# Performance work log

Measured on AMD Instinct MI355X. Metric: run time of the kernel, lower is better.

## Reference

```python
import jax, jax.numpy as jnp
import numpy as np

B, K, D = 8192, 8192, 512


def setup_inputs() -> dict:
    key = jax.random.key(0)
    k1, k2 = jax.random.split(key)
    previous_residual = jax.random.normal(k1, (B, D), dtype=jnp.float32)
    codebook_embeddings = jax.random.normal(k2, (K, D), dtype=jnp.float32)
    return {"previous_residual": previous_residual,
            "codebook_embeddings": codebook_embeddings}


def reference(previous_residual, codebook_embeddings):
    # Squared Euclidean distances [B, K] via the expansion
    # subtract+square+sum, without materializing the [B, K, D] intermediate).
    x_sq = jnp.sum(previous_residual * previous_residual, axis=-1, keepdims=True)   # [B, 1]
    e_sq = jnp.sum(codebook_embeddings * codebook_embeddings, axis=-1)              # [K]
    cross = jnp.einsum('bd,kd->bk', previous_residual, codebook_embeddings)         # [B, K]
    distances = x_sq - 2.0 * cross + e_sq[None, :]                                  # [B, K]
    closest_codebook_index = jnp.argmin(distances, axis=1)                          # [B] int
    codebook_embedding = codebook_embeddings[closest_codebook_index]                # [B, D] gather
    next_residual = previous_residual - codebook_embedding                          # [B, D]
    return closest_codebook_index, next_residual
```

## Files before the change

kernel.cpp:

```cpp
#include <hip/hip_runtime.h>

#define Bn 8192
#define Kn 8192
#define Dn 512
#define WINDOW 0.25f

typedef _Float16 half8 __attribute__((ext_vector_type(8)));
typedef float floatx4 __attribute__((ext_vector_type(4)));
typedef unsigned long long u64;

__device__ __forceinline__ unsigned int fkey(float f) {
    unsigned int u = __float_as_uint(f);
    return (u & 0x80000000u) ? ~u : (u | 0x80000000u);
}

__device__ __forceinline__ void gld16(const _Float16* g, _Float16* l) {
    __builtin_amdgcn_global_load_lds(
        (const __attribute__((address_space(1))) unsigned int*)g,
        (__attribute__((address_space(3))) unsigned int*)l, 16, 0, 0);
}

__global__ __launch_bounds__(256) void esq_kernel(const float* __restrict__ E,
                                                  float* __restrict__ esq) {
    int wave = threadIdx.x >> 6;
    int lane = threadIdx.x & 63;
    int k = blockIdx.x * 4 + wave;
    const float4* row = (const float4*)(E + (size_t)k * Dn);
    float4 v0 = row[lane];
    float4 v1 = row[64 + lane];
    float s = v0.x*v0.x + v0.y*v0.y + v0.z*v0.z + v0.w*v0.w
            + v1.x*v1.x + v1.y*v1.y + v1.z*v1.z + v1.w*v1.w;
    #pragma unroll
    for (int off = 32; off > 0; off >>= 1) s += __shfl_down(s, off, 64);
    if (lane == 0) esq[k] = s;
}

__global__ __launch_bounds__(256) void convert_hi(
    const float* __restrict__ X, const float* __restrict__ E,
    _Float16* __restrict__ Xh, _Float16* __restrict__ Eh,
    float* __restrict__ esq)
{
    const bool isE = blockIdx.x >= 1024;
    const int pc = blockIdx.x & 1023;
    const int panel = pc >> 4;
    const int chunk = pc & 15;
    const float* src = isE ? E : X;
    _Float16* dst = isE ? Eh : Xh;
    const int t = threadIdx.x;
    const int row = t >> 1;
    const int kh  = (t & 1) * 16;
    const float* p = &src[(size_t)(panel * 128 + row) * Dn + chunk * 32 + kh];
    float4 v[4];
    v[0] = *(const float4*)(p + 0);
    v[1] = *(const float4*)(p + 4);
    v[2] = *(const float4*)(p + 8);
    v[3] = *(const float4*)(p + 12);
    const int slotbase = ((row >> 6) << 8) + (((row >> 4) & 3) << 6) + (row & 15);
    #pragma unroll
    for (int j = 0; j < 2; ++j) {
        half8 h;
        #pragma unroll
        for (int q = 0; q < 2; ++q) {
            const float4 w = v[j * 2 + q];
            h[q*4+0]=(_Float16)w.x; h[q*4+1]=(_Float16)w.y;
            h[q*4+2]=(_Float16)w.z; h[q*4+3]=(_Float16)w.w;
        }
        const int kq = (t & 1) * 2 + j;
        const size_t off = ((size_t)(panel * 16 + chunk) * 512
                            + slotbase + kq * 16) * 8;
        *(half8*)&dst[off] = h;
    }
    if (isE) {
        float s = 0.f;
        #pragma unroll
        for (int i = 0; i < 4; ++i)
            s += v[i].x*v[i].x + v[i].y*v[i].y + v[i].z*v[i].z + v[i].w*v[i].w;
        s += __shfl_xor(s, 1);
        if ((t & 1) == 0) atomicAdd(&esq[panel * 128 + row], s);
    }
}

__global__ __launch_bounds__(256, 2) void argmin_hi(
    const _Float16* __restrict__ Xh, const _Float16* __restrict__ Eh,
    const float* __restrict__ esq, float* __restrict__ bestf)
{
    __shared__ __align__(16) _Float16 sX[2][8192];
    __shared__ __align__(16) _Float16 sE[2][8192];

    const int tid  = threadIdx.x;
    const int bid  = blockIdx.x;
    const int lid  = bid >> 3;
    const int rg   = (bid & 7) | ((lid & 1) << 3);
    const int mb   = lid >> 1;
    const int m0   = mb * 128, n0 = rg * 512;
    const int lane = tid & 63, wave = tid >> 6;
    const int wx   = wave & 1, wy = wave >> 1;
    const int colg = lane & 15, quad = lane >> 4;

    float v1[16], v2[16];
    #pragma unroll
    for (int i = 0; i < 16; ++i) { v1[i] = INFINITY; v2[i] = INFINITY; }

    const _Float16* gX  = Xh + (size_t)mb * 65536 + tid * 8;
    const _Float16* gE0 = Eh + (size_t)(rg * 4) * 65536 + tid * 8;
    const int aoff = wy * 2048 + lane * 8;
    const int boff = wx * 2048 + lane * 8;
    const unsigned colg4 = (unsigned)colg << 4;

    auto stage = [&](int cc, int b) {
        const _Float16* sx = gX + (cc & 7) * 8192;
        const _Float16* se = gE0 + (size_t)(cc >> 3) * 65536 + (cc & 7) * 8192;
        _Float16* dX = &sX[b][tid * 8];
        _Float16* dE = &sE[b][tid * 8];
        #pragma unroll
        for (int j = 0; j < 4; ++j) gld16(sx + j * 2048, dX + j * 2048);
        #pragma unroll
        for (int j = 0; j < 4; ++j) gld16(se + j * 2048, dE + j * 2048);
    };

    floatx4 acc[4][4];

    auto compute = [&](int b) {
        #pragma unroll
        for (int s = 0; s < 2; ++s) {
            const int so = s * 4096;
            half8 bh[4];
            #pragma unroll
            for (int ni = 0; ni < 4; ++ni)
                bh[ni] = *(const half8*)&sE[b][boff + so + ni * 512];
            #pragma unroll
            for (int mi = 0; mi < 4; ++mi) {
                half8 ah = *(const half8*)&sX[b][aoff + so + mi * 512];
                #pragma unroll
                for (int ni = 0; ni < 4; ++ni)
                    acc[mi][ni] = __builtin_amdgcn_mfma_f32_16x16x32_f16(
                        ah, bh[ni], acc[mi][ni], 0, 0, 0);
            }
        }
    };

    stage(0, 0);
    asm volatile("s_waitcnt vmcnt(0)" ::: "memory");
    __builtin_amdgcn_s_barrier();

    for (int nt = 0; nt < 4; ++nt) {
        #pragma unroll
        for (int i = 0; i < 4; ++i)
            #pragma unroll
            for (int j = 0; j < 4; ++j) acc[i][j] = {0.f, 0.f, 0.f, 0.f};

        for (int c2 = 0; c2 < 4; ++c2) {
            const int cc0 = nt * 8 + c2 * 2;
            stage(cc0 + 1, 1);
            compute(0);
            asm volatile("s_waitcnt vmcnt(0)" ::: "memory");
            __builtin_amdgcn_s_barrier();
            if (cc0 + 2 < 32) stage(cc0 + 2, 0);
            compute(1);
            asm volatile("s_waitcnt vmcnt(0)" ::: "memory");
            __builtin_amdgcn_s_barrier();
        }

        float eqv[4];
        #pragma unroll
        for (int ni = 0; ni < 4; ++ni)
            eqv[ni] = esq[n0 + nt * 128 + wx * 64 + ni * 16 + colg];
        #pragma unroll
        for (int mi = 0; mi < 4; ++mi)
            #pragma unroll
            for (int r = 0; r < 4; ++r) {
                const int i = mi * 4 + r;
                #pragma unroll
                for (int ni = 0; ni < 4; ++ni) {
                    const float dv = eqv[ni] - 2.0f * acc[mi][ni][r];
                    const unsigned ob = colg4 | (unsigned)((nt << 2) | ni);
                    const float key = __uint_as_float(
                        (__float_as_uint(dv) & 0xFFFFFF00u) | ob);
                    v2[i] = fminf(v2[i], fmaxf(v1[i], key));
                    v1[i] = fminf(v1[i], key);
                }
            }
    }

    #pragma unroll
    for (int mi = 0; mi < 4; ++mi)
        #pragma unroll
        for (int r = 0; r < 4; ++r) {
            const int i = mi * 4 + r;
            float a1 = v1[i], a2 = v2[i];
            #pragma unroll
            for (int off = 1; off < 16; off <<= 1) {
                const float p1 = __shfl_xor(a1, off);
                const float p2 = __shfl_xor(a2, off);
                a2 = fminf(fmaxf(a1, p1), fminf(a2, p2));
                a1 = fminf(a1, p1);
            }
            if (colg == 0) {
                const int row = m0 + wy * 64 + mi * 16 + quad * 4 + r;
                float2 st; st.x = a1; st.y = a2;
                *(float2*)&bestf[(size_t)row * 64 + rg * 4 + wx * 2] = st;
            }
        }
}

__global__ __launch_bounds__(256) void refine_kernel(
    const float* __restrict__ X, const float* __restrict__ E,
    const float* __restrict__ bestf, float* __restrict__ out)
{
    const int lane = threadIdx.x & 63, wave = threadIdx.x >> 6;
    const int b = blockIdx.x * 4 + wave;

    const float val = bestf[(size_t)b * 64 + lane];
    const unsigned bits = __float_as_uint(val);
    const int rg = lane >> 2, wx = (lane >> 1) & 1;
    const int colg = (bits >> 4) & 15, nt = (bits >> 2) & 3, ni = bits & 3;
    const int col = rg * 512 + nt * 128 + wx * 64 + ni * 16 + colg;

    float mn = val;
    #pragma unroll
    for (int off = 1; off < 64; off <<= 1) mn = fminf(mn, __shfl_xor(mn, off));

    const float4* xr = (const float4*)(X + (size_t)b * Dn);
    const float4 x0 = xr[lane * 2], x1 = xr[lane * 2 + 1];

    u64 bestk = ~0ull;
    u64 mask = __ballot(val <= mn + WINDOW);
    while (mask) {
        const int s = __builtin_ctzll(mask);
        mask &= mask - 1;
        const int c = __shfl(col, s);
        const float4* er = (const float4*)(E + (size_t)c * Dn);
        const float4 e0 = er[lane * 2], e1 = er[lane * 2 + 1];
        float p = e0.x*(e0.x - 2.f*x0.x) + e0.y*(e0.y - 2.f*x0.y)
                + e0.z*(e0.z - 2.f*x0.z) + e0.w*(e0.w - 2.f*x0.w)
                + e1.x*(e1.x - 2.f*x1.x) + e1.y*(e1.y - 2.f*x1.y)
                + e1.z*(e1.z - 2.f*x1.z) + e1.w*(e1.w - 2.f*x1.w);
        #pragma unroll
        for (int off = 1; off < 64; off <<= 1) p += __shfl_xor(p, off);
        const u64 k = ((u64)fkey(p) << 32) | (u64)(unsigned int)c;
        if (k < bestk) bestk = k;
    }

    const int idx = (int)(unsigned int)(bestk & 0xFFFFFFFFull);
    if (lane == 0) out[b] = (float)idx;
    const float4* er = (const float4*)(E + (size_t)idx * Dn);
    const float4 e0 = er[lane * 2], e1 = er[lane * 2 + 1];
    float4 r0, r1;
    r0.x = x0.x - e0.x; r0.y = x0.y - e0.y; r0.z = x0.z - e0.z; r0.w = x0.w - e0.w;
    r1.x = x1.x - e1.x; r1.y = x1.y - e1.y; r1.z = x1.z - e1.z; r1.w = x1.w - e1.w;
    float4* o = (float4*)(out + Bn + (size_t)b * Dn);
    o[lane * 2] = r0; o[lane * 2 + 1] = r1;
}

#define KSPLIT 16
#define LDSW 132
__global__ __launch_bounds__(256, 2) void argmin_fp32(
    const float* __restrict__ X, const float* __restrict__ E,
    const float* __restrict__ esq, u64* __restrict__ best)
{
    __shared__ __align__(16) float Xs[16][LDSW];
    __shared__ __align__(16) float Es[16][LDSW];
    __shared__ u64 red[128][16];
    const int tid = threadIdx.x;
    const int tx = tid & 15, ty = tid >> 4;
    const int rowTile = blockIdx.x / KSPLIT;
    const int split   = blockIdx.x % KSPLIT;
    const int m0 = rowTile * 128;
    const int kbase = split * (Kn / KSPLIT);
    float bestv[8]; int besti[8];
    #pragma unroll
    for (int i = 0; i < 8; ++i) { bestv[i] = INFINITY; besti[i] = 0; }
    const int ldRow = tid >> 2, ldD = (tid & 3) * 4;
    for (int kt = 0; kt < (Kn / KSPLIT) / 128; ++kt) {
        const int k0 = kbase + kt * 128;
        float acc[8][8] = {};
        for (int dc = 0; dc < Dn / 16; ++dc) {
            const int d0 = dc * 16;
            float4 xa = *(const float4*)&X[(size_t)(m0 + ldRow)      * Dn + d0 + ldD];
            float4 xb = *(const float4*)&X[(size_t)(m0 + 64 + ldRow) * Dn + d0 + ldD];
            float4 ea = *(const float4*)&E[(size_t)(k0 + ldRow)      * Dn + d0 + ldD];
            float4 eb = *(const float4*)&E[(size_t)(k0 + 64 + ldRow) * Dn + d0 + ldD];
            __syncthreads();
            Xs[ldD+0][ldRow] = xa.x; Xs[ldD+1][ldRow] = xa.y;
            Xs[ldD+2][ldRow] = xa.z; Xs[ldD+3][ldRow] = xa.w;
            Xs[ldD+0][64+ldRow] = xb.x; Xs[ldD+1][64+ldRow] = xb.y;
            Xs[ldD+2][64+ldRow] = xb.z; Xs[ldD+3][64+ldRow] = xb.w;
            Es[ldD+0][ldRow] = ea.x; Es[ldD+1][ldRow] = ea.y;
            Es[ldD+2][ldRow] = ea.z; Es[ldD+3][ldRow] = ea.w;
            Es[ldD+0][64+ldRow] = eb.x; Es[ldD+1][64+ldRow] = eb.y;
            Es[ldD+2][64+ldRow] = eb.z; Es[ldD+3][64+ldRow] = eb.w;
            __syncthreads();
            #pragma unroll
            for (int d = 0; d < 16; ++d) {
                float a8[8], b8[8];
                *(float4*)&a8[0] = *(const float4*)&Xs[d][4*ty];
                *(float4*)&a8[4] = *(const float4*)&Xs[d][64 + 4*ty];
                *(float4*)&b8[0] = *(const float4*)&Es[d][4*tx];
                *(float4*)&b8[4] = *(const float4*)&Es[d][64 + 4*tx];
                #pragma unroll
                for (int i = 0; i < 8; ++i)
                    #pragma unroll
                    for (int j = 0; j < 8; ++j) acc[i][j] += a8[i] * b8[j];
            }
        }
        #pragma unroll
        for (int j = 0; j < 8; ++j) {
            const int c = k0 + ((j < 4) ? (4*tx + j) : (64 + 4*tx + (j - 4)));
            const float eq = esq[c];
            #pragma unroll
            for (int i = 0; i < 8; ++i) {
                float dval = eq - 2.0f * acc[i][j];
                if (dval < bestv[i]) { bestv[i] = dval; besti[i] = c; }
            }
        }
    }
    #pragma unroll
    for (int i = 0; i < 8; ++i) {
        int rloc = (i < 4) ? (4*ty + i) : (64 + 4*ty + (i - 4));
        red[rloc][tx] = ((u64)fkey(bestv[i]) << 32) | (u64)(unsigned int)besti[i];
    }
    __syncthreads();
    if (tid < 128) {
        u64 m = red[tid][0];
        #pragma unroll
        for (int t = 1; t < 16; ++t) { u64 v = red[tid][t]; if (v < m) m = v; }
        best[(size_t)(m0 + tid) * KSPLIT + split] = m;
    }
}

__global__ __launch_bounds__(256) void finalize_kernel(
    const float* __restrict__ X, const float* __restrict__ E,
    const u64* __restrict__ best, float* __restrict__ out, int nsplits)
{
    __shared__ int sidx[2];
    const int half = threadIdx.x >> 7;
    const int t    = threadIdx.x & 127;
    const int b    = blockIdx.x * 2 + half;
    if (t < 64) {
        u64 v = (t < nsplits) ? best[(size_t)b * nsplits + t] : ~0ull;
        #pragma unroll
        for (int off = 1; off < 64; off <<= 1) {
            u64 o = __shfl_xor(v, off);
            if (o < v) v = o;
        }
        if (t == 0) {
            int idx = (int)(unsigned int)(v & 0xFFFFFFFFull);
            sidx[half] = idx;
            out[b] = (float)idx;
        }
    }
    __syncthreads();
    const int idx = sidx[half];
    float4 x = ((const float4*)(X + (size_t)b * Dn))[t];
    float4 e = ((const float4*)(E + (size_t)idx * Dn))[t];
    float4 r; r.x = x.x - e.x; r.y = x.y - e.y; r.z = x.z - e.z; r.w = x.w - e.w;
    ((float4*)(out + Bn + (size_t)b * Dn))[t] = r;
}

extern "C" void kernel_launch(void* const* d_in, const int* in_sizes, int n_in,
                              void* d_out, int out_size, void* d_ws, size_t ws_size,
                              hipStream_t stream) {
    const float* X = (const float*)d_in[0];
    const float* E = (const float*)d_in[1];
    float* out = (float*)d_out;

    const size_t HB = (size_t)Bn * Dn * sizeof(_Float16);
    const size_t BESTB = (size_t)Bn * 64 * sizeof(float);
    const size_t NEED = 32768 + 2 * HB + BESTB;

    float* esq = (float*)d_ws;

    if (ws_size >= NEED) {
        _Float16* Xh = (_Float16*)((char*)d_ws + 32768);
        _Float16* Eh = (_Float16*)((char*)d_ws + 32768 + HB);
        float* bestf = (float*)((char*)d_ws + 32768 + 2 * HB);
        hipMemsetAsync((void*)esq, 0, Kn * sizeof(float), stream);
        convert_hi<<<2048, 256, 0, stream>>>(X, E, Xh, Eh, esq);
        argmin_hi<<<64 * 16, 256, 0, stream>>>(Xh, Eh, esq, bestf);
        refine_kernel<<<Bn / 4, 256, 0, stream>>>(X, E, bestf, out);
    } else {
        u64* best = (u64*)((char*)d_ws + 32768);
        esq_kernel<<<Kn / 4, 256, 0, stream>>>(E, esq);
        argmin_fp32<<<(Bn / 128) * KSPLIT, 256, 0, stream>>>(X, E, esq, best);
        finalize_kernel<<<Bn / 2, 256, 0, stream>>>(X, E, best, out, KSPLIT);
    }
}
```

Before: 177.2 us.

## Retile fp16 argmin GEMM to 256x256 blocks with 8 waves and finer pipelining

The distance GEMM kernel now uses 512-thread blocks covering 256 rows by 256 codebook columns with the full K=512 depth. Each wave holds a 128x64 accumulator tile (8x4 MFMA tiles) instead of looping over four 128-column subtiles. The double-buffered LDS staging is split into half-chunk loads interleaved with MFMA groups using partial vmcnt waits and s_setprio. Top-2 candidates are reduced across waves through LDS before being written, and the refine kernel's column decode is updated to the new layout. The larger tile is meant to increase data reuse and cut global/LDS traffic per FLOP. In exchange it raises register pressure from 128 accumulator floats per lane, which could hurt occupancy.

```diff
diff --git a/kernel.cpp b/kernel.cpp
--- a/kernel.cpp
+++ b/kernel.cpp
@@ -80,127 +80,161 @@
     }
 }
 
-__global__ __launch_bounds__(256, 2) void argmin_hi(
+__global__ __launch_bounds__(512, 2) void argmin_hi(
     const _Float16* __restrict__ Xh, const _Float16* __restrict__ Eh,
     const float* __restrict__ esq, float* __restrict__ bestf)
 {
-    __shared__ __align__(16) _Float16 sX[2][8192];
-    __shared__ __align__(16) _Float16 sE[2][8192];
+    __shared__ __align__(16) _Float16 sA[2][2][2][4096];
+    __shared__ __align__(16) _Float16 sB[2][2][2][4096];
 
     const int tid  = threadIdx.x;
     const int bid  = blockIdx.x;
-    const int lid  = bid >> 3;
-    const int rg   = (bid & 7) | ((lid & 1) << 3);
-    const int mb   = lid >> 1;
-    const int m0   = mb * 128, n0 = rg * 512;
+    const int bx   = bid & 31;
+    const int by   = bid >> 5;
     const int lane = tid & 63, wave = tid >> 6;
-    const int wx   = wave & 1, wy = wave >> 1;
+    const int wm   = wave >> 2;
+    const int wn   = wave & 3;
     const int colg = lane & 15, quad = lane >> 4;
 
-    float v1[16], v2[16];
-    #pragma unroll
-    for (int i = 0; i < 16; ++i) { v1[i] = INFINITY; v2[i] = INFINITY; }
-
-    const _Float16* gX  = Xh + (size_t)mb * 65536 + tid * 8;
-    const _Float16* gE0 = Eh + (size_t)(rg * 4) * 65536 + tid * 8;
-    const int aoff = wy * 2048 + lane * 8;
-    const int boff = wx * 2048 + lane * 8;
-    const unsigned colg4 = (unsigned)colg << 4;
-
-    auto stage = [&](int cc, int b) {
-        const _Float16* sx = gX + (cc & 7) * 8192;
-        const _Float16* se = gE0 + (size_t)(cc >> 3) * 65536 + (cc & 7) * 8192;
-        _Float16* dX = &sX[b][tid * 8];
-        _Float16* dE = &sE[b][tid * 8];
-        #pragma unroll
-        for (int j = 0; j < 4; ++j) gld16(sx + j * 2048, dX + j * 2048);
-        #pragma unroll
-        for (int j = 0; j < 4; ++j) gld16(se + j * 2048, dE + j * 2048);
+    const _Float16* gA = Xh + (size_t)(2 * by) * 65536 + tid * 8;
+    const _Float16* gB = Eh + (size_t)(2 * bx) * 65536 + tid * 8;
+
+    auto stgA = [&](int t, int kh, int b) {
+        const int c = (2 * t + kh) * 4096;
+        gld16(gA + c,         &sA[b][kh][0][tid * 8]);
+        gld16(gA + 65536 + c, &sA[b][kh][1][tid * 8]);
     };
-
-    floatx4 acc[4][4];
-
-    auto compute = [&](int b) {
-        #pragma unroll
-        for (int s = 0; s < 2; ++s) {
-            const int so = s * 4096;
-            half8 bh[4];
+    auto stgB = [&](int t, int kh, int b) {
+        const int c = (2 * t + kh) * 4096;
+        gld16(gB + c,         &sB[b][kh][0][tid * 8]);
+        gld16(gB + 65536 + c, &sB[b][kh][1][tid * 8]);
+    };
+
+    floatx4 acc[8][4];
+    #pragma unroll
+    for (int i = 0; i < 8; ++i)
+        #pragma unroll
+        for (int j = 0; j < 4; ++j) acc[i][j] = {0.f, 0.f, 0.f, 0.f};
+
+    stgA(0, 0, 0); stgB(0, 0, 0); stgA(0, 1, 0); stgB(0, 1, 0);
+
+    const int la8 = lane * 8;
+    const int bo  = (wn & 1) * 2048 + la8;
+
+    for (int t = 0; t < 8; ++t) {
+        const int b = t & 1, nb = b ^ 1;
+        const bool pf = (t < 7);
+        const _Float16* A0 = &sA[b][0][wm][0];
+        const _Float16* A1 = &sA[b][1][wm][0];
+        const _Float16* B0 = &sB[b][0][wn >> 1][bo];
+        const _Float16* B1 = &sB[b][1][wn >> 1][bo];
+        half8 a[4], bb[4];
+
+        asm volatile("s_waitcnt vmcnt(4)" ::: "memory");
+        __builtin_amdgcn_s_barrier();
+
+        #pragma unroll
+        for (int ni = 0; ni < 4; ++ni) bb[ni] = *(const half8*)&B0[ni * 512];
+        #pragma unroll
+        for (int i = 0; i < 4; ++i)   a[i]  = *(const half8*)&A0[i * 512 + la8];
+        if (pf) stgA(t + 1, 0, nb);
+        __builtin_amdgcn_s_setprio(1);
+        #pragma unroll
+        for (int i = 0; i < 4; ++i)
             #pragma unroll
             for (int ni = 0; ni < 4; ++ni)
-                bh[ni] = *(const half8*)&sE[b][boff + so + ni * 512];
-            #pragma unroll
-            for (int mi = 0; mi < 4; ++mi) {
-                half8 ah = *(const half8*)&sX[b][aoff + so + mi * 512];
-                #pragma unroll
-                for (int ni = 0; ni < 4; ++ni)
-                    acc[mi][ni] = __builtin_amdgcn_mfma_f32_16x16x32_f16(
-                        ah, bh[ni], acc[mi][ni], 0, 0, 0);
+                acc[i][ni] = __builtin_amdgcn_mfma_f32_16x16x32_f16(
+                    a[i], bb[ni], acc[i][ni], 0, 0, 0);
+        __builtin_amdgcn_s_setprio(0);
+
+        #pragma unroll
+        for (int i = 0; i < 4; ++i) a[i] = *(const half8*)&A0[2048 + i * 512 + la8];
+        if (pf) stgB(t + 1, 0, nb);
+        __builtin_amdgcn_s_setprio(1);
+        #pragma unroll
+        for (int i = 0; i < 4; ++i)
+            #pragma unroll
+            for (int ni = 0; ni < 4; ++ni)
+                acc[4 + i][ni] = __builtin_amdgcn_mfma_f32_16x16x32_f16(
+                    a[i], bb[ni], acc[4 + i][ni], 0, 0, 0);
+        __builtin_amdgcn_s_setprio(0);
+
+        if (pf) asm volatile("s_waitcnt vmcnt(4)" ::: "memory");
+        else    asm volatile("s_waitcnt vmcnt(0)" ::: "memory");
+        __builtin_amdgcn_s_barrier();
+
+        #pragma unroll
+        for (int ni = 0; ni < 4; ++ni) bb[ni] = *(const half8*)&B1[ni * 512];
+        #pragma unroll
+        for (int i = 0; i < 4; ++i)   a[i]  = *(const half8*)&A1[i * 512 + la8];
+        if (pf) stgA(t + 1, 1, nb);
+        __builtin_amdgcn_s_setprio(1);
+        #pragma unroll
+        for (int i = 0; i < 4; ++i)
+            #pragma unroll
+            for (int ni = 0; ni < 4; ++ni)
+                acc[i][ni] = __builtin_amdgcn_mfma_f32_16x16x32_f16(
+                    a[i], bb[ni], acc[i][ni], 0, 0, 0);
+        __builtin_amdgcn_s_setprio(0);
+
+        #pragma unroll
+        for (int i = 0; i < 4; ++i) a[i] = *(const half8*)&A1[2048 + i * 512 + la8];
+        if (pf) stgB(t + 1, 1, nb);
+        __builtin_amdgcn_s_setprio(1);
+        #pragma unroll
+        for (int i = 0; i < 4; ++i)
+            #pragma unroll
+            for (int ni = 0; ni < 4; ++ni)
+                acc[4 + i][ni] = __builtin_amdgcn_mfma_f32_16x16x32_f16(
+                    a[i], bb[ni], acc[4 + i][ni], 0, 0, 0);
+        __builtin_amdgcn_s_setprio(0);
+    }
+
+    float2* sm = (float2*)&sA[0][0][0][0];
+    const int n0 = bx * 256 + wn * 64;
+    float eqv[4];
+    #pragma unroll
+    for (int ni = 0; ni < 4; ++ni) eqv[ni] = esq[n0 + ni * 16 + colg];
+    const unsigned ob_base = ((unsigned)colg << 4) | ((unsigned)wn << 2);
+
+    #pragma unroll
+    for (int mi = 0; mi < 8; ++mi)
+        #pragma unroll
+        for (int r = 0; r < 4; ++r) {
+            float w1 = INFINITY, w2 = INFINITY;
+            #pragma unroll
+            for (int ni = 0; ni < 4; ++ni) {
+                const float dv = eqv[ni] - 2.0f * acc[mi][ni][r];
+                const float key = __uint_as_float(
+                    (__float_as_uint(dv) & 0xFFFFFF00u) | (ob_base | (unsigned)ni));
+                w2 = fminf(w2, fmaxf(w1, key));
+                w1 = fminf(w1, key);
             }
-        }
-    };
-
-    stage(0, 0);
-    asm volatile("s_waitcnt vmcnt(0)" ::: "memory");
-    __builtin_amdgcn_s_barrier();
-
-    for (int nt = 0; nt < 4; ++nt) {
-        #pragma unroll
-        for (int i = 0; i < 4; ++i)
-            #pragma unroll
-            for (int j = 0; j < 4; ++j) acc[i][j] = {0.f, 0.f, 0.f, 0.f};
-
-        for (int c2 = 0; c2 < 4; ++c2) {
-            const int cc0 = nt * 8 + c2 * 2;
-            stage(cc0 + 1, 1);
-            compute(0);
-            asm volatile("s_waitcnt vmcnt(0)" ::: "memory");
-            __builtin_amdgcn_s_barrier();
-            if (cc0 + 2 < 32) stage(cc0 + 2, 0);
-            compute(1);
-            asm volatile("s_waitcnt vmcnt(0)" ::: "memory");
-            __builtin_amdgcn_s_barrier();
-        }
-
-        float eqv[4];
-        #pragma unroll
-        for (int ni = 0; ni < 4; ++ni)
-            eqv[ni] = esq[n0 + nt * 128 + wx * 64 + ni * 16 + colg];
-        #pragma unroll
-        for (int mi = 0; mi < 4; ++mi)
-            #pragma unroll
-            for (int r = 0; r < 4; ++r) {
-                const int i = mi * 4 + r;
-                #pragma unroll
-                for (int ni = 0; ni < 4; ++ni) {
-                    const float dv = eqv[ni] - 2.0f * acc[mi][ni][r];
-                    const unsigned ob = colg4 | (unsigned)((nt << 2) | ni);
-                    const float key = __uint_as_float(
-                        (__float_as_uint(dv) & 0xFFFFFF00u) | ob);
-                    v2[i] = fminf(v2[i], fmaxf(v1[i], key));
-                    v1[i] = fminf(v1[i], key);
-                }
-            }
-    }
-
-    #pragma unroll
-    for (int mi = 0; mi < 4; ++mi)
-        #pragma unroll
-        for (int r = 0; r < 4; ++r) {
-            const int i = mi * 4 + r;
-            float a1 = v1[i], a2 = v2[i];
             #pragma unroll
             for (int off = 1; off < 16; off <<= 1) {
-                const float p1 = __shfl_xor(a1, off);
-                const float p2 = __shfl_xor(a2, off);
-                a2 = fminf(fmaxf(a1, p1), fminf(a2, p2));
-                a1 = fminf(a1, p1);
+                const float p1 = __shfl_xor(w1, off);
+                const float p2 = __shfl_xor(w2, off);
+                w2 = fminf(fmaxf(w1, p1), fminf(w2, p2));
+                w1 = fminf(w1, p1);
             }
             if (colg == 0) {
-                const int row = m0 + wy * 64 + mi * 16 + quad * 4 + r;
-                float2 st; st.x = a1; st.y = a2;
-                *(float2*)&bestf[(size_t)row * 64 + rg * 4 + wx * 2] = st;
+                const int row128 = mi * 16 + quad * 4 + r;
+                float2 st; st.x = w1; st.y = w2;
+                sm[(wm * 128 + row128) * 4 + wn] = st;
             }
         }
+    __syncthreads();
+    if (tid < 256) {
+        float m1 = INFINITY, m2 = INFINITY;
+        #pragma unroll
+        for (int w = 0; w < 4; ++w) {
+            const float2 p = sm[tid * 4 + w];
+            m2 = fminf(fmaxf(m1, p.x), fminf(m2, p.y));
+            m1 = fminf(m1, p.x);
+        }
+        float2 st; st.x = m1; st.y = m2;
+        *(float2*)&bestf[(size_t)(by * 256 + tid) * 64 + bx * 2] = st;
+    }
 }
 
 __global__ __launch_bounds__(256) void refine_kernel(
@@ -212,9 +246,9 @@
 
     const float val = bestf[(size_t)b * 64 + lane];
     const unsigned bits = __float_as_uint(val);
-    const int rg = lane >> 2, wx = (lane >> 1) & 1;
-    const int colg = (bits >> 4) & 15, nt = (bits >> 2) & 3, ni = bits & 3;
-    const int col = rg * 512 + nt * 128 + wx * 64 + ni * 16 + colg;
+    const int cb = lane >> 1;
+    const int colg = (bits >> 4) & 15, wn = (bits >> 2) & 3, ni = bits & 3;
+    const int col = cb * 256 + wn * 64 + ni * 16 + colg;
 
     float mn = val;
     #pragma unroll
@@ -376,7 +410,7 @@
         float* bestf = (float*)((char*)d_ws + 32768 + 2 * HB);
         hipMemsetAsync((void*)esq, 0, Kn * sizeof(float), stream);
         convert_hi<<<2048, 256, 0, stream>>>(X, E, Xh, Eh, esq);
-        argmin_hi<<<64 * 16, 256, 0, stream>>>(Xh, Eh, esq, bestf);
+        argmin_hi<<<1024, 512, 0, stream>>>(Xh, Eh, esq, bestf);
         refine_kernel<<<Bn / 4, 256, 0, stream>>>(X, E, bestf, out);
     } else {
         u64* best = (u64*)((char*)d_ws + 32768);
```

Result: no change. 179.0 us (+1.0%).
